# Kernel tuning notes

Hardware: AMD Instinct MI355X
Metric: run time of the kernel (lower is better)

## Reference

```python
import jax, jax.numpy as jnp
import numpy as np

N_CODES = 512
D = 8
BETA = 0.25


def setup_inputs() -> dict:
    key = jax.random.key(0)
    k1, k2 = jax.random.split(key)
    z = jax.random.normal(k1, (8, D, 16, 64, 64), dtype=jnp.float32)
    # torch init: uniform(-1/n_codes, 1/n_codes)
    codebook = jax.random.uniform(
        k2, (N_CODES, D), dtype=jnp.float32,
        minval=-1.0 / N_CODES, maxval=1.0 / N_CODES)
    return {"z": z, "codebook": codebook}


def reference(z, codebook):
    B, Dc, T, H, W = z.shape
    # [B, T, H, W, D] -> [N, D]
    z_flat = jnp.transpose(z, (0, 2, 3, 4, 1)).reshape(-1, Dc)
    z2 = jnp.sum(z_flat * z_flat, axis=1, keepdims=True)          # [N, 1]
    e2 = jnp.sum(codebook * codebook, axis=1)[None, :]            # [1, K]
    ze = z_flat @ codebook.T                                      # [N, K]
    dists = z2 + e2 - 2.0 * ze
    idx = jnp.argmin(dists, axis=1)                               # [N]
    z_q = jnp.transpose(codebook[idx].reshape(B, T, H, W, Dc), (0, 4, 1, 2, 3))
    commit = jnp.mean((jax.lax.stop_gradient(z_q) - z) ** 2)
    codebk = jnp.mean((z_q - jax.lax.stop_gradient(z)) ** 2)
    vq_loss = codebk + BETA * commit
    z_q_st = z + jax.lax.stop_gradient(z_q - z)
    return z_q_st, vq_loss, idx.reshape(B, T, H, W)
```

## Files before the change

### kernel.cpp

```cpp
#include <hip/hip_runtime.h>


#define NPTS      524288
#define KCODES    512
#define DDIM      8
#define CH_STRIDE 65536
#define B_STRIDE  524288
#define BLK       512
#define NWAVES    8
#define NTILES    32
#define CMAX      4
#define FLT_BIG   3.402823466e+38f

typedef short bf8 __attribute__((ext_vector_type(8)));
typedef float f4  __attribute__((ext_vector_type(4)));

__device__ __forceinline__ unsigned short f2bf(float f) {
    unsigned u = __float_as_uint(f);
    unsigned r = u + 0x7fffu + ((u >> 16) & 1u);
    return (unsigned short)(r >> 16);
}
__device__ __forceinline__ float bf2f(unsigned short h) {
    return __uint_as_float(((unsigned)h) << 16);
}

__device__ __forceinline__ float np_sumsq8(const float* x) {
    float p0 = __fmul_rn(x[0], x[0]);
    float p1 = __fmul_rn(x[1], x[1]);
    float p2 = __fmul_rn(x[2], x[2]);
    float p3 = __fmul_rn(x[3], x[3]);
    float p4 = __fmul_rn(x[4], x[4]);
    float p5 = __fmul_rn(x[5], x[5]);
    float p6 = __fmul_rn(x[6], x[6]);
    float p7 = __fmul_rn(x[7], x[7]);
    return __fadd_rn(__fadd_rn(__fadd_rn(p0, p1), __fadd_rn(p2, p3)),
                     __fadd_rn(__fadd_rn(p4, p5), __fadd_rn(p6, p7)));
}

__device__ __forceinline__ float np_dist(const float* __restrict__ cb,
                                         const float* __restrict__ e2f,
                                         int k, const float* zv, float z2) {
    const float* c = cb + (size_t)k * DDIM;
    float ze = 0.0f;
    #pragma unroll
    for (int j = 0; j < DDIM; ++j) ze = __fmaf_rn(zv[j], c[j], ze);
    return __fmaf_rn(-2.0f, ze, __fadd_rn(z2, e2f[k]));
}

__global__ void prep(const float* __restrict__ cb, float* __restrict__ e2f,
                     unsigned short* __restrict__ wsB, float* __restrict__ out_loss) {
    const int tid = blockIdx.x * 256 + threadIdx.x;
    if (tid == 0) *out_loss = 0.0f;
    const int t    = tid >> 6;
    const int lane = tid & 63;
    const int quad = lane >> 4;
    const int colc = lane & 15;
    const int n    = t * 16 + colc;
    float row[DDIM];
    #pragma unroll
    for (int j = 0; j < DDIM; ++j) row[j] = cb[n * DDIM + j];
    const float e2 = np_sumsq8(row);
    if (quad == 3) e2f[n] = e2;

    unsigned short sh[8];
    #pragma unroll
    for (int j = 0; j < 8; ++j) {
        const unsigned short eh = f2bf(row[j]);
        const unsigned short el = f2bf(__fsub_rn(row[j], bf2f(eh)));
        sh[j] = (quad == 1) ? el : eh;
    }
    if (quad == 3) {
        const unsigned short e2h = f2bf(e2);
        const unsigned short e2l = f2bf(__fsub_rn(e2, bf2f(e2h)));
        sh[0] = e2h; sh[1] = e2l;
        #pragma unroll
        for (int j = 2; j < 8; ++j) sh[j] = 0;
    }
    unsigned short* dst = wsB + (size_t)(t * 64 + lane) * 8;
    #pragma unroll
    for (int j = 0; j < 8; ++j) dst[j] = sh[j];
}

__global__ __launch_bounds__(BLK, 4) void vq_main(
    const float* __restrict__ z, const float* __restrict__ cb,
    const float* __restrict__ e2f, const unsigned short* __restrict__ wsB,
    float* __restrict__ out_zq, float* __restrict__ out_loss,
    float* __restrict__ out_idx)
{
    __shared__ unsigned short ldsB[NTILES * 64 * 8];
    __shared__ int            ccnt[BLK];
    __shared__ unsigned short clist[BLK][CMAX];
    __shared__ float          wsum[NWAVES];

    const int tid  = threadIdx.x;
    const int wave = tid >> 6;
    const int lane = tid & 63;
    const int quad = lane >> 4;
    const int col  = lane & 15;

    {
        const uint4* src = (const uint4*)wsB;
        uint4* dst = (uint4*)ldsB;
        #pragma unroll
        for (int q = 0; q < 4; ++q)
            dst[tid + q * BLK] = src[tid + q * BLK];
    }
    ccnt[tid] = 0;

    const int n = blockIdx.x * BLK + tid;
    const int b = n >> 16;
    const int s = n & 65535;
    const float* zp = z + (size_t)b * B_STRIDE + s;
    float zv[DDIM];
    #pragma unroll
    for (int j = 0; j < DDIM; ++j) zv[j] = zp[(size_t)j * CH_STRIDE];
    const float z2 = np_sumsq8(zv);

    float zmax = z2;
    #pragma unroll
    for (int mk = 1; mk <= 32; mk <<= 1) zmax = fmaxf(zmax, __shfl_xor(zmax, mk, 64));
    const float eps = zmax * 6e-7f + 3e-6f;

    unsigned pkz[8];
    #pragma unroll
    for (int j = 0; j < 8; ++j) {
        const unsigned short hh = f2bf(zv[j]);
        const float zh = bf2f(hh);
        const float zl = __fsub_rn(zv[j], zh);
        const unsigned short ah = f2bf(-2.0f * zh);
        const unsigned short al = f2bf(-2.0f * zl);
        pkz[j] = (unsigned)ah | ((unsigned)al << 16);
    }

    bf8 af0, af1, af2, af3;
#define MK_AFRAG(AF, Q)                                                        \
    {                                                                          \
        const int srcl = (Q)*16 + col;                                         \
        _Pragma("unroll")                                                      \
        for (int j = 0; j < 8; ++j) {                                          \
            const unsigned w = (unsigned)__shfl((int)pkz[j], srcl, 64);        \
            const unsigned us = (quad == 2) ? (w >> 16) : (w & 0xFFFFu);       \
            AF[j] = (short)us;                                                 \
        }                                                                      \
        if (quad == 3) AF = (bf8){(short)0x3F80, (short)0x3F80, 0, 0, 0, 0, 0, 0}; \
    }
    MK_AFRAG(af0, 0) MK_AFRAG(af1, 1) MK_AFRAG(af2, 2) MK_AFRAG(af3, 3)

    __syncthreads();

    const bf8* __restrict__ Bp = (const bf8*)ldsB;

    f4 mn0 = (f4){FLT_BIG, FLT_BIG, FLT_BIG, FLT_BIG};
    f4 mn1 = mn0, mn2 = mn0, mn3 = mn0;
    #pragma unroll 4
    for (int t = 0; t < NTILES; ++t) {
        const bf8 bfrag = Bp[t * 64 + lane];
        f4 zero = (f4){0.0f, 0.0f, 0.0f, 0.0f};
        const f4 a0 = __builtin_amdgcn_mfma_f32_16x16x32_bf16(af0, bfrag, zero, 0, 0, 0);
        const f4 a1 = __builtin_amdgcn_mfma_f32_16x16x32_bf16(af1, bfrag, zero, 0, 0, 0);
        const f4 a2 = __builtin_amdgcn_mfma_f32_16x16x32_bf16(af2, bfrag, zero, 0, 0, 0);
        const f4 a3 = __builtin_amdgcn_mfma_f32_16x16x32_bf16(af3, bfrag, zero, 0, 0, 0);
        #pragma unroll
        for (int r = 0; r < 4; ++r) {
            mn0[r] = fminf(mn0[r], a0[r]); mn1[r] = fminf(mn1[r], a1[r]);
            mn2[r] = fminf(mn2[r], a2[r]); mn3[r] = fminf(mn3[r], a3[r]);
        }
    }
    #pragma unroll
    for (int mk = 1; mk <= 8; mk <<= 1) {
        #pragma unroll
        for (int r = 0; r < 4; ++r) {
            mn0[r] = fminf(mn0[r], __shfl_xor(mn0[r], mk, 64));
            mn1[r] = fminf(mn1[r], __shfl_xor(mn1[r], mk, 64));
            mn2[r] = fminf(mn2[r], __shfl_xor(mn2[r], mk, 64));
            mn3[r] = fminf(mn3[r], __shfl_xor(mn3[r], mk, 64));
        }
    }
    #pragma unroll
    for (int r = 0; r < 4; ++r) {
        mn0[r] += eps; mn1[r] += eps; mn2[r] += eps; mn3[r] += eps;
    }

    const int pbase = wave * 64 + quad * 4;
    #pragma unroll 4
    for (int t = 0; t < NTILES; ++t) {
        const bf8 bfrag = Bp[t * 64 + lane];
        f4 zero = (f4){0.0f, 0.0f, 0.0f, 0.0f};
        const f4 a0 = __builtin_amdgcn_mfma_f32_16x16x32_bf16(af0, bfrag, zero, 0, 0, 0);
        const f4 a1 = __builtin_amdgcn_mfma_f32_16x16x32_bf16(af1, bfrag, zero, 0, 0, 0);
        const f4 a2 = __builtin_amdgcn_mfma_f32_16x16x32_bf16(af2, bfrag, zero, 0, 0, 0);
        const f4 a3 = __builtin_amdgcn_mfma_f32_16x16x32_bf16(af3, bfrag, zero, 0, 0, 0);
        const unsigned short code = (unsigned short)(t * 16 + col);
#define PUSH(AQ, MQ, Q)                                                        \
    {                                                                          \
        const bool c0 = AQ[0] <= MQ[0], c1 = AQ[1] <= MQ[1];                   \
        const bool c2 = AQ[2] <= MQ[2], c3 = AQ[3] <= MQ[3];                   \
        if (c0 | c1 | c2 | c3) {                                               \
            const int pt = pbase + (Q)*16;                                     \
            if (c0) { int p = atomicAdd(&ccnt[pt + 0], 1); if (p < CMAX) clist[pt + 0][p] = code; } \
            if (c1) { int p = atomicAdd(&ccnt[pt + 1], 1); if (p < CMAX) clist[pt + 1][p] = code; } \
            if (c2) { int p = atomicAdd(&ccnt[pt + 2], 1); if (p < CMAX) clist[pt + 2][p] = code; } \
            if (c3) { int p = atomicAdd(&ccnt[pt + 3], 1); if (p < CMAX) clist[pt + 3][p] = code; } \
        }                                                                      \
    }
        PUSH(a0, mn0, 0) PUSH(a1, mn1, 1) PUSH(a2, mn2, 2) PUSH(a3, mn3, 3)
    }

    asm volatile("s_waitcnt lgkmcnt(0)" ::: "memory");

    const int cnt = ccnt[tid];
    int bidx;
    if (cnt == 1) {
        bidx = clist[tid][0];
    } else if (cnt <= CMAX) {
        float best = FLT_BIG; bidx = 0;
        for (int i = 0; i < cnt; ++i) {
            const int k = clist[tid][i];
            const float d = np_dist(cb, e2f, k, zv, z2);
            if (d < best || (d == best && k < bidx)) { best = d; bidx = k; }
        }
    } else {
        float best = FLT_BIG; bidx = 0;
        for (int k = 0; k < KCODES; ++k) {
            const float d = np_dist(cb, e2f, k, zv, z2);
            if (d < best) { best = d; bidx = k; }
        }
    }
    out_idx[n] = (float)bidx;

    const float* cw = cb + (size_t)bidx * DDIM;
    float* op = out_zq + (size_t)b * B_STRIDE + s;
    float lsum = 0.0f;
    #pragma unroll
    for (int j = 0; j < DDIM; ++j) {
        const float zq = cw[j];
        const float t  = __fsub_rn(zq, zv[j]);
        op[(size_t)j * CH_STRIDE] = __fadd_rn(zv[j], t);
        lsum = __fmaf_rn(t, t, lsum);
    }

    #pragma unroll
    for (int off = 32; off > 0; off >>= 1) lsum += __shfl_down(lsum, off, 64);
    if (lane == 0) wsum[wave] = lsum;
    __syncthreads();
    if (tid == 0) {
        float bs = 0.0f;
        #pragma unroll
        for (int w = 0; w < NWAVES; ++w) bs += wsum[w];
        atomicAdd(out_loss, bs * (1.25f / 4194304.0f));
    }
}

extern "C" void kernel_launch(void* const* d_in, const int* in_sizes, int n_in,
                              void* d_out, int out_size, void* d_ws, size_t ws_size,
                              hipStream_t stream) {
    const float* z  = (const float*)d_in[0];
    const float* cb = (const float*)d_in[1];
    float* out      = (float*)d_out;
    float* out_zq   = out;
    float* out_loss = out + 4194304;
    float* out_idx  = out + 4194305;
    float* e2f            = (float*)d_ws;
    unsigned short* wsB   = (unsigned short*)((char*)d_ws + 2048);

    prep<<<8, 256, 0, stream>>>(cb, e2f, wsB, out_loss);
    vq_main<<<NPTS / BLK, BLK, 0, stream>>>(z, cb, e2f, wsB,
                                            out_zq, out_loss, out_idx);
}
```

Baseline: 119.5 us.

## Fuse codebook prep into main kernel and shrink LDS B-fragment layout

Removes the separate prep kernel: each block now converts the codebook to split bf16 hi/lo fragments plus e2 directly into LDS, and the exact-distance fallback recomputes e2 from the codebook row instead of reading a precomputed array. The LDS layout drops the duplicated hi rows (48 instead of 64 entries per tile), with a per-lane remap so quads 0 and 2 share the hi row. The loss zeroing moves to a hipMemsetAsync. This saves a kernel launch and dependency, and cuts LDS use, at the cost of redundant per-block conversion work and an extra memset node.

```diff
diff --git a/kernel.cpp b/kernel.cpp
--- a/kernel.cpp
+++ b/kernel.cpp
@@ -37,57 +37,25 @@
                      __fadd_rn(__fadd_rn(p4, p5), __fadd_rn(p6, p7)));
 }
 
-__device__ __forceinline__ float np_dist(const float* __restrict__ cb,
-                                         const float* __restrict__ e2f,
-                                         int k, const float* zv, float z2) {
+__device__ __forceinline__ float np_dist_cb(const float* __restrict__ cb,
+                                            int k, const float* zv, float z2) {
     const float* c = cb + (size_t)k * DDIM;
+    float cr[DDIM];
+    #pragma unroll
+    for (int j = 0; j < DDIM; ++j) cr[j] = c[j];
     float ze = 0.0f;
     #pragma unroll
-    for (int j = 0; j < DDIM; ++j) ze = __fmaf_rn(zv[j], c[j], ze);
-    return __fmaf_rn(-2.0f, ze, __fadd_rn(z2, e2f[k]));
-}
-
-__global__ void prep(const float* __restrict__ cb, float* __restrict__ e2f,
-                     unsigned short* __restrict__ wsB, float* __restrict__ out_loss) {
-    const int tid = blockIdx.x * 256 + threadIdx.x;
-    if (tid == 0) *out_loss = 0.0f;
-    const int t    = tid >> 6;
-    const int lane = tid & 63;
-    const int quad = lane >> 4;
-    const int colc = lane & 15;
-    const int n    = t * 16 + colc;
-    float row[DDIM];
-    #pragma unroll
-    for (int j = 0; j < DDIM; ++j) row[j] = cb[n * DDIM + j];
-    const float e2 = np_sumsq8(row);
-    if (quad == 3) e2f[n] = e2;
-
-    unsigned short sh[8];
-    #pragma unroll
-    for (int j = 0; j < 8; ++j) {
-        const unsigned short eh = f2bf(row[j]);
-        const unsigned short el = f2bf(__fsub_rn(row[j], bf2f(eh)));
-        sh[j] = (quad == 1) ? el : eh;
-    }
-    if (quad == 3) {
-        const unsigned short e2h = f2bf(e2);
-        const unsigned short e2l = f2bf(__fsub_rn(e2, bf2f(e2h)));
-        sh[0] = e2h; sh[1] = e2l;
-        #pragma unroll
-        for (int j = 2; j < 8; ++j) sh[j] = 0;
-    }
-    unsigned short* dst = wsB + (size_t)(t * 64 + lane) * 8;
-    #pragma unroll
-    for (int j = 0; j < 8; ++j) dst[j] = sh[j];
+    for (int j = 0; j < DDIM; ++j) ze = __fmaf_rn(zv[j], cr[j], ze);
+    const float e2 = np_sumsq8(cr);
+    return __fmaf_rn(-2.0f, ze, __fadd_rn(z2, e2));
 }
 
 __global__ __launch_bounds__(BLK, 4) void vq_main(
     const float* __restrict__ z, const float* __restrict__ cb,
-    const float* __restrict__ e2f, const unsigned short* __restrict__ wsB,
     float* __restrict__ out_zq, float* __restrict__ out_loss,
     float* __restrict__ out_idx)
 {
-    __shared__ unsigned short ldsB[NTILES * 64 * 8];
+    __shared__ unsigned short ldsB[NTILES * 48 * 8];
     __shared__ int            ccnt[BLK];
     __shared__ unsigned short clist[BLK][CMAX];
     __shared__ float          wsum[NWAVES];
@@ -99,11 +67,31 @@
     const int col  = lane & 15;
 
     {
-        const uint4* src = (const uint4*)wsB;
-        uint4* dst = (uint4*)ldsB;
-        #pragma unroll
-        for (int q = 0; q < 4; ++q)
-            dst[tid + q * BLK] = src[tid + q * BLK];
+        const float* row = cb + (size_t)tid * DDIM;
+        float rv[DDIM];
+        #pragma unroll
+        for (int j = 0; j < DDIM; ++j) rv[j] = row[j];
+        const float e2 = np_sumsq8(rv);
+
+        unsigned eh2[4], el2[4];
+        #pragma unroll
+        for (int jj = 0; jj < 4; ++jj) {
+            const unsigned short h0 = f2bf(rv[2 * jj]);
+            const unsigned short h1 = f2bf(rv[2 * jj + 1]);
+            const unsigned short l0 = f2bf(__fsub_rn(rv[2 * jj],     bf2f(h0)));
+            const unsigned short l1 = f2bf(__fsub_rn(rv[2 * jj + 1], bf2f(h1)));
+            eh2[jj] = (unsigned)h0 | ((unsigned)h1 << 16);
+            el2[jj] = (unsigned)l0 | ((unsigned)l1 << 16);
+        }
+        const unsigned short e2h = f2bf(e2);
+        const unsigned short e2l = f2bf(__fsub_rn(e2, bf2f(e2h)));
+
+        const int t = tid >> 4;
+        const int c = tid & 15;
+        uint4* base = (uint4*)ldsB;
+        base[t * 48 + c]      = (uint4){eh2[0], eh2[1], eh2[2], eh2[3]};
+        base[t * 48 + 16 + c] = (uint4){el2[0], el2[1], el2[2], el2[3]};
+        base[t * 48 + 32 + c] = (uint4){(unsigned)e2h | ((unsigned)e2l << 16), 0u, 0u, 0u};
     }
     ccnt[tid] = 0;
 
@@ -148,13 +136,14 @@
 
     __syncthreads();
 
+    const int rl = lane - ((quad == 2) ? 32 : ((quad == 3) ? 16 : 0));
     const bf8* __restrict__ Bp = (const bf8*)ldsB;
 
     f4 mn0 = (f4){FLT_BIG, FLT_BIG, FLT_BIG, FLT_BIG};
     f4 mn1 = mn0, mn2 = mn0, mn3 = mn0;
     #pragma unroll 4
     for (int t = 0; t < NTILES; ++t) {
-        const bf8 bfrag = Bp[t * 64 + lane];
+        const bf8 bfrag = Bp[t * 48 + rl];
         f4 zero = (f4){0.0f, 0.0f, 0.0f, 0.0f};
         const f4 a0 = __builtin_amdgcn_mfma_f32_16x16x32_bf16(af0, bfrag, zero, 0, 0, 0);
         const f4 a1 = __builtin_amdgcn_mfma_f32_16x16x32_bf16(af1, bfrag, zero, 0, 0, 0);
@@ -184,7 +173,7 @@
     const int pbase = wave * 64 + quad * 4;
     #pragma unroll 4
     for (int t = 0; t < NTILES; ++t) {
-        const bf8 bfrag = Bp[t * 64 + lane];
+        const bf8 bfrag = Bp[t * 48 + rl];
         f4 zero = (f4){0.0f, 0.0f, 0.0f, 0.0f};
         const f4 a0 = __builtin_amdgcn_mfma_f32_16x16x32_bf16(af0, bfrag, zero, 0, 0, 0);
         const f4 a1 = __builtin_amdgcn_mfma_f32_16x16x32_bf16(af1, bfrag, zero, 0, 0, 0);
@@ -216,13 +205,13 @@
         float best = FLT_BIG; bidx = 0;
         for (int i = 0; i < cnt; ++i) {
             const int k = clist[tid][i];
-            const float d = np_dist(cb, e2f, k, zv, z2);
+            const float d = np_dist_cb(cb, k, zv, z2);
             if (d < best || (d == best && k < bidx)) { best = d; bidx = k; }
         }
     } else {
         float best = FLT_BIG; bidx = 0;
         for (int k = 0; k < KCODES; ++k) {
-            const float d = np_dist(cb, e2f, k, zv, z2);
+            const float d = np_dist_cb(cb, k, zv, z2);
             if (d < best) { best = d; bidx = k; }
         }
     }
@@ -260,10 +249,7 @@
     float* out_zq   = out;
     float* out_loss = out + 4194304;
     float* out_idx  = out + 4194305;
-    float* e2f            = (float*)d_ws;
-    unsigned short* wsB   = (unsigned short*)((char*)d_ws + 2048);
-
-    prep<<<8, 256, 0, stream>>>(cb, e2f, wsB, out_loss);
-    vq_main<<<NPTS / BLK, BLK, 0, stream>>>(z, cb, e2f, wsB,
-                                            out_zq, out_loss, out_idx);
-}
+
+    hipMemsetAsync(out_loss, 0, sizeof(float), stream);
+    vq_main<<<NPTS / BLK, BLK, 0, stream>>>(z, cb, out_zq, out_loss, out_idx);
+}
```

Result: no change. 119.8 us (+0.3%).
